# Optimization experiments

Measured on AMD Instinct MI355X. Metric: run time of the kernel, lower is better.

Reference implementation:

```python
import jax, jax.numpy as jnp
import numpy as np

SEQ_LEN, BATCH, HIDDEN, OUT = 512, 4096, 2048, 10


def setup_inputs() -> dict:
    key = jax.random.key(0)
    ks = jax.random.split(key, 7)
    return {
        "x": jax.random.normal(ks[0], (SEQ_LEN, BATCH), jnp.float32),
        "Wx": jax.random.normal(ks[1], (HIDDEN, 1), jnp.float32) * 0.05,
        "bx": jax.random.normal(ks[2], (HIDDEN,), jnp.float32) * 0.05,
        "Wh": jax.random.normal(ks[3], (1, HIDDEN), jnp.float32) * 0.05,
        "bh": jax.random.normal(ks[4], (1,), jnp.float32) * 0.05,
        "Wy": jax.random.normal(ks[5], (OUT, HIDDEN), jnp.float32) * 0.05,
        "by": jax.random.normal(ks[6], (OUT,), jnp.float32) * 0.05,
    }


def reference(x, Wx, bx, Wh, bh, Wy, by):
    # x: [T, B]; input_dim == 1 structurally (torch code reshapes x[i] to (B, 1)).
    B = x.shape[1]
    H = Wx.shape[0]
    wx = Wx[:, 0]  # [H]

    def step(h, xt):
        # linear_x(x_t): (B,1) @ (1,H) -> outer product, [B, H]
        x_out = xt[:, None] * wx[None, :] + bx
        # linear_h(h): [B, H] @ [H, 1] -> [B, 1], broadcasts into the add (as in torch)
        h_out = h @ Wh.T + bh
        h_new = jnp.tanh(x_out + h_out)
        return h_new, None

    h0 = jnp.zeros((B, H), x.dtype)
    h_final, _ = jax.lax.scan(step, h0, x)
    logits = h_final @ Wy.T + by  # [B, OUT]
    return jax.nn.softmax(logits, axis=-1)
```

## Files before the change

### kernel.cpp

```cpp
#include <hip/hip_runtime.h>
#include <math.h>


#define SEQ   512
#define BATCH 4096
#define HID   2048
#define NOUT  10
#define KPL   32
#define ROWQ  9

#define NS    560
#define S_LOc   (-10.0f)
#define S_H     (20.0f / 559.0f)
#define S_INVH  (559.0f / 20.0f)
#define S_BIAS  (10.0f * S_INVH)
#define NSM1F   559.0f
#define DZ14    43.0f
#define DZ9     69.875f
#define NSA     1120
#define NSAM1F  1119.0f
#define NSAM2F  1118.0f
#define S_HA    (20.0f / 1119.0f)
#define S_INVHA (1119.0f / 20.0f)
#define S_BIASA (10.0f * S_INVHA)
#define DZA     (1119.0f / 13.0f)
#define UPS_ALPHA (1119.0f / 559.0f)
#define U_SCALE (8.0f / 14.0f)
#define U_BIAS  4.0f
#define UCMAXF  7.99951f

#define TABLE_FLOATS (NS * ROWQ * 4)
#define WSA_FLOATS (4096 + 14 * 4096)
#define WSB_FLOATS (4096 + 4 * 4096)
#define WS3_FLOATS (57344 + 57344 + 4096 + 20160)

__device__ __forceinline__ float fast_exp2(float v) { return __builtin_amdgcn_exp2f(v); }
__device__ __forceinline__ float fast_rcp(float v)  { return __builtin_amdgcn_rcpf(v); }
__device__ __forceinline__ float med3(float a, float lo, float hi) {
    return __builtin_amdgcn_fmed3f(a, lo, hi);
}
__device__ __forceinline__ float fast_tanh(float a) {
    const float C = 2.8853900817779268f;
    return __builtin_fmaf(-2.0f, fast_rcp(fast_exp2(C * a) + 1.0f), 1.0f);
}
__device__ __forceinline__ float wave_sum(float v) {
#pragma unroll
    for (int m = 1; m < 64; m <<= 1) v += __shfl_xor(v, m, 64);
    return v;
}
__device__ __forceinline__ float combine_eval(float z, int nn, float dz,
                                              const float* baseA, const float* baseB,
                                              int split, int b) {
    float p = z / dz;
    int   c = min(max((int)floorf(p) - 1, 0), nn - 4);
    float t = p - (float)c;
    float a0 = t, a1 = t - 1.0f, a2 = t - 2.0f, a3 = t - 3.0f;
    float m01 = a0 * a1, m23 = a2 * a3;
    float w0 = a1 * m23 * (-1.0f / 6.0f), w1 = a0 * m23 * 0.5f;
    float w2 = m01 * a3 * (-0.5f),        w3 = m01 * a2 * (1.0f / 6.0f);
    float y[4];
#pragma unroll
    for (int i = 0; i < 4; ++i) {
        int n = c + i;
        const float* ptr = (n < split) ? (baseA + (size_t)n * 4096)
                                       : (baseB + (size_t)(n - split) * 4096);
        y[i] = ptr[b];
    }
    return __builtin_fmaf(w0, y[0], w1 * y[1]) + __builtin_fmaf(w2, y[2], w3 * y[3]);
}

__global__ __launch_bounds__(256) void k_coef(const float* __restrict__ Wx, const float* __restrict__ bx,
                                              const float* __restrict__ Wh, const float* __restrict__ bh,
                                              float* __restrict__ tab_g,
                                              float s_h, float s_invh, float s_bias) {
    __shared__ float red[256];
    __shared__ float Gn[32];
    const int k    = blockIdx.x;
    const int node = threadIdx.x & 31;
    const int jc   = threadIdx.x >> 5;
    const int cell = node >> 2, nn = node & 3;
    const float sn = S_LOc + (float)k * s_h;
    const float xi_n = (nn == 0) ? 0.923879533f : (nn == 1) ? 0.382683432f
                     : (nn == 2) ? -0.382683432f : -0.923879533f;
    const float un = (-7.0f + ((float)cell + 0.5f) * 1.75f) + 0.875f * xi_n;
    float p = 0.0f;
    const int j0 = jc * 256;
#pragma unroll 4
    for (int j = j0; j < j0 + 256; ++j)
        p += Wh[j] * fast_tanh(__builtin_fmaf(Wx[j], un, bx[j] + sn));
    red[threadIdx.x] = p;
    __syncthreads();
    if (threadIdx.x < 32) {
        float V = bh[0];
#pragma unroll
        for (int c = 0; c < 8; ++c) V += red[threadIdx.x + 32 * c];
        Gn[threadIdx.x] = __builtin_fmaf(V, s_invh, s_bias);
    }
    __syncthreads();
    float4* wq = (float4*)tab_g;
    if (threadIdx.x < 8) {
        const int c = threadIdx.x;
        float G0 = Gn[4*c+0], G1 = Gn[4*c+1], G2 = Gn[4*c+2], G3 = Gn[4*c+3];
        float d03 = G0 - G3, d12 = G1 - G2;
        float a0 = 0.25f * (G0 + G1 + G2 + G3);
        float a1 = 0.5f * (0.923879533f * d03 + 0.382683432f * d12);
        float a2 = 0.5f * 0.707106781f * (G0 - G1 - G2 + G3);
        float a3 = 0.5f * (0.382683432f * d03 - 0.923879533f * d12);
        wq[k * ROWQ + c] = make_float4(a0 - a2, a1 - 3.0f * a3, 2.0f * a2, 4.0f * a3);
    } else if (threadIdx.x == 8) {
        wq[k * ROWQ + 8] = make_float4(0.f, 0.f, 0.f, 0.f);
    }
}

__global__ __launch_bounds__(256) void k_upsample(const float* __restrict__ src,
                                                  float* __restrict__ dst) {
    const int idx = blockIdx.x * 256 + threadIdx.x;
    if (idx >= NSA * ROWQ) return;
    const int r = idx / 9;
    const int c = idx - r * 9;
    float4* d4 = (float4*)dst;
    if (c == 8) { d4[idx] = make_float4(0.f, 0.f, 0.f, 0.f); return; }
    float z5 = (float)r * (559.0f / 1119.0f);
    float kf = med3(floorf(z5) - 1.0f, 0.0f, 556.0f);
    int   k  = (int)kf;
    float t  = z5 - kf;
    float a0 = t, a1 = t - 1.0f, a2 = t - 2.0f, a3 = t - 3.0f;
    float m01 = a0 * a1, m23 = a2 * a3;
    float w0 = a1 * m23 * (-1.0f / 6.0f), w1 = a0 * m23 * 0.5f;
    float w2 = m01 * a3 * (-0.5f),        w3 = m01 * a2 * (1.0f / 6.0f);
    const float4* s4 = (const float4*)src;
    float4 y0 = s4[(k    ) * 9 + c];
    float4 y1 = s4[(k + 1) * 9 + c];
    float4 y2 = s4[(k + 2) * 9 + c];
    float4 y3 = s4[(k + 3) * 9 + c];
    float4 o;
    o.x = UPS_ALPHA * (w0 * y0.x + w1 * y1.x + w2 * y2.x + w3 * y3.x);
    o.y = UPS_ALPHA * (w0 * y0.y + w1 * y1.y + w2 * y2.y + w3 * y3.y);
    o.z = UPS_ALPHA * (w0 * y0.z + w1 * y1.z + w2 * y2.z + w3 * y3.z);
    o.w = UPS_ALPHA * (w0 * y0.w + w1 * y1.w + w2 * y2.w + w3 * y3.w);
    d4[idx] = o;
}

__global__ __launch_bounds__(256) void k_scan3(const float* __restrict__ x,
                                               const float* __restrict__ bh,
                                               const float* __restrict__ tab_g,
                                               float* __restrict__ z170,
                                               float* __restrict__ buf1,
                                               float* __restrict__ buf2) {
    __shared__ float4 tabs[NSA * ROWQ];
    {
        const float4* src = (const float4*)tab_g;
        for (int i = threadIdx.x; i < NSA * ROWQ; i += 256) tabs[i] = src[i];
    }
    __syncthreads();
    const int ptype = blockIdx.x >> 4;
    const int chunk = blockIdx.x & 15;
    const int b     = chunk * 256 + threadIdx.x;
    const int seg   = (ptype == 0) ? 0 : ((ptype <= 7) ? 1 : 2);
    const int nA    = (seg == 1) ? 2 * (ptype - 1) : ((seg == 2) ? 2 * (ptype - 8) : 0);
    const int nB    = nA + 1;

    const int t0     = (seg == 0) ? 0 : ((seg == 1) ? 170 : 340);
    const int nsteps = (seg == 2) ? 171 : 170;

    const float z0 = med3(__builtin_fmaf(bh[0], S_INVHA, S_BIASA), 0.0f, NSAM1F);
    float zA = (seg == 0) ? z0 : (float)nA * DZA;
    float zB = (seg == 0) ? z0 : (float)nB * DZA;

    auto step_pair = [&](float xi, float xi2, int ci) {
        float kfA = med3(zA, 0.0f, NSAM2F);
        float kfB = med3(zB, 0.0f, NSAM2F);
        int   kA  = (int)kfA;
        int   kB  = (int)kfB;
        int   ia  = ((kA << 3) + kA) + ci;
        int   ib  = ((kB << 3) + kB) + ci;
        float4 qa0 = tabs[ia];
        float4 qa1 = tabs[ia + ROWQ];
        float4 qb0 = tabs[ib];
        float4 qb1 = tabs[ib + ROWQ];
        float tA = med3(zA, 0.0f, NSAM1F) - (float)kA;
        float tB = med3(zB, 0.0f, NSAM1F) - (float)kB;
        float la0 = __builtin_fmaf(qa0.y, xi, qa0.x), ha0 = __builtin_fmaf(qa0.w, xi, qa0.z);
        float la1 = __builtin_fmaf(qa1.y, xi, qa1.x), ha1 = __builtin_fmaf(qa1.w, xi, qa1.z);
        float ra0 = __builtin_fmaf(ha0, xi2, la0);
        float ra1 = __builtin_fmaf(ha1, xi2, la1);
        zA = __builtin_fmaf(tA, ra1 - ra0, ra0);
        float lb0 = __builtin_fmaf(qb0.y, xi, qb0.x), hb0 = __builtin_fmaf(qb0.w, xi, qb0.z);
        float lb1 = __builtin_fmaf(qb1.y, xi, qb1.x), hb1 = __builtin_fmaf(qb1.w, xi, qb1.z);
        float rb0 = __builtin_fmaf(hb0, xi2, lb0);
        float rb1 = __builtin_fmaf(hb1, xi2, lb1);
        zB = __builtin_fmaf(tB, rb1 - rb0, rb0);
    };

    float cur[8], nxt[8];
#pragma unroll
    for (int i = 0; i < 8; ++i)
        cur[i] = x[(size_t)min(t0 + i, SEQ - 1) * BATCH + b];

    const int full = nsteps >> 3, tail = nsteps & 7;
    for (int c = 0; c < full; ++c) {
        const int nb = t0 + (c + 1) * 8;
#pragma unroll
        for (int i = 0; i < 8; ++i)
            nxt[i] = x[(size_t)min(nb + i, SEQ - 1) * BATCH + b];
        float xiA[8], xi2A[8]; int ciA[8];
#pragma unroll
        for (int i = 0; i < 8; ++i) {
            float uc = med3(__builtin_fmaf(cur[i], U_SCALE, U_BIAS), 0.0f, UCMAXF);
            int   ci = (int)uc;
            float xi = __builtin_fmaf(2.0f, uc - (float)ci, -1.0f);
            xiA[i] = xi; xi2A[i] = xi * xi; ciA[i] = ci;
        }
#pragma unroll
        for (int i = 0; i < 8; ++i) step_pair(xiA[i], xi2A[i], ciA[i]);
#pragma unroll
        for (int i = 0; i < 8; ++i) cur[i] = nxt[i];
    }
    for (int i = 0; i < tail; ++i) {
        float uc = med3(__builtin_fmaf(cur[i], U_SCALE, U_BIAS), 0.0f, UCMAXF);
        int   ci = (int)uc;
        float xi = __builtin_fmaf(2.0f, uc - (float)ci, -1.0f);
        step_pair(xi, xi * xi, ci);
    }

    if (seg == 0) {
        z170[b] = zA;
    } else if (seg == 1) {
        buf1[(size_t)nA * 4096 + b] = zA;
        buf1[(size_t)nB * 4096 + b] = zB;
    } else {
        buf2[(size_t)nA * 4096 + b] = zA;
        buf2[(size_t)nB * 4096 + b] = zB;
    }
}

__global__ __launch_bounds__(256) void head3(
    const float* __restrict__ x,  const float* __restrict__ Wx,
    const float* __restrict__ bx, const float* __restrict__ Wy,
    const float* __restrict__ by, const float* __restrict__ z170,
    const float* __restrict__ buf1, const float* __restrict__ buf2,
    float* __restrict__ out)
{
    const int lane = threadIdx.x & 63;
    const int wave = threadIdx.x >> 6;
    const int b    = blockIdx.x * 4 + wave;

    float z340 = combine_eval(z170[b], 14, DZA, buf1, buf1, 14, b);
    z340 = med3(z340, 0.0f, NSAM1F);
    float z511 = combine_eval(z340, 14, DZA, buf2, buf2, 14, b);
    const float s = __builtin_fmaf(z511, S_HA, S_LOc);

    const float C  = 2.8853900817779268f;
    const float u  = x[(size_t)(SEQ - 1) * BATCH + b];
    const float sc = s * C;
    float acc[NOUT];
#pragma unroll
    for (int i = 0; i < NOUT; ++i) acc[i] = 0.0f;
#pragma unroll 4
    for (int k = 0; k < KPL; ++k) {
        const int j = k * 64 + lane;
        float arg = __builtin_fmaf(u, Wx[j] * C, bx[j] * C) + sc;
        float r   = fast_rcp(fast_exp2(arg) + 1.0f);
        float th  = __builtin_fmaf(-2.0f, r, 1.0f);
#pragma unroll
        for (int i = 0; i < NOUT; ++i)
            acc[i] = __builtin_fmaf(Wy[i * HID + j], th, acc[i]);
    }
#pragma unroll
    for (int i = 0; i < NOUT; ++i) acc[i] = wave_sum(acc[i]) + by[i];
    float m = acc[0];
#pragma unroll
    for (int i = 1; i < NOUT; ++i) m = fmaxf(m, acc[i]);
    const float L2E = 1.4426950408889634f;
    float ev[NOUT]; float Z = 0.0f;
#pragma unroll
    for (int i = 0; i < NOUT; ++i) { ev[i] = fast_exp2((acc[i] - m) * L2E); Z += ev[i]; }
    const float rz = fast_rcp(Z);
    if (lane == 0) {
#pragma unroll
        for (int i = 0; i < NOUT; ++i) out[(size_t)b * NOUT + i] = ev[i] * rz;
    }
}

__global__ __launch_bounds__(256) void k_scan_quad(const float* __restrict__ x,
                                                   const float* __restrict__ bh,
                                                   const float* __restrict__ tab_g,
                                                   float* __restrict__ z255,
                                                   float* __restrict__ baseA,
                                                   float* __restrict__ baseB,
                                                   int split, float dz) {
    __shared__ float4 tabs[5200];
    {
        const float4* src = (const float4*)tab_g;
        for (int i = threadIdx.x; i < NS * ROWQ; i += 256) tabs[i] = src[i];
    }
    __syncthreads();
    const int blk = blockIdx.x;
    const int seg  = (blk < 16) ? 0 : 1;
    const int node = seg ? (blk - 16) >> 4 : 0;
    const int eb   = seg ? (blk - 16) & 15 : blk;
    const int b    = eb * 256 + threadIdx.x;

    const int t0     = seg ? 255 : 0;
    const int nsteps = seg ? 256 : 255;

    float za = seg ? (float)node * dz
                   : med3(__builtin_fmaf(bh[0], S_INVH, S_BIAS), 0.0f, NSM1F);

    auto step1 = [&](float xi, float xi2, int cim) {
        float mm  = med3(za + 0.5f, 1.0f, 558.0f);
        int   km  = (int)mm;
        int   idx = ((km << 3) + km) + cim;
        float4 qm = tabs[idx];
        float4 q0 = tabs[idx + ROWQ];
        float4 qp = tabs[idx + 2 * ROWQ];
        float kmf = (float)km;
        float zc  = med3(za, 0.0f, NSM1F);
        float t   = zc - kmf;
        float wm  = 0.5f * t * (t - 1.0f);
        float wp  = 0.5f * t * (t + 1.0f);
        float w0  = 1.0f - t * t;
        float lm = __builtin_fmaf(qm.y, xi, qm.x), hm = __builtin_fmaf(qm.w, xi, qm.z);
        float l0 = __builtin_fmaf(q0.y, xi, q0.x), h0 = __builtin_fmaf(q0.w, xi, q0.z);
        float lp = __builtin_fmaf(qp.y, xi, qp.x), hp = __builtin_fmaf(qp.w, xi, qp.z);
        float rm = __builtin_fmaf(hm, xi2, lm);
        float r0 = __builtin_fmaf(h0, xi2, l0);
        float rp = __builtin_fmaf(hp, xi2, lp);
        za = __builtin_fmaf(wm, rm, w0 * r0) + wp * rp;
    };

    float cur[8], nxt[8];
#pragma unroll
    for (int i = 0; i < 8; ++i)
        cur[i] = x[(size_t)min(t0 + i, SEQ - 1) * BATCH + b];

    const int full = nsteps >> 3, tail = nsteps & 7;
    for (int c = 0; c < full; ++c) {
        const int nb = t0 + (c + 1) * 8;
#pragma unroll
        for (int i = 0; i < 8; ++i)
            nxt[i] = x[(size_t)min(nb + i, SEQ - 1) * BATCH + b];
        float xiA[8], xi2A[8]; int cimA[8];
#pragma unroll
        for (int i = 0; i < 8; ++i) {
            float uc = med3(__builtin_fmaf(cur[i], U_SCALE, U_BIAS), 0.0f, UCMAXF);
            int   ci = (int)uc;
            float xi = __builtin_fmaf(2.0f, uc - (float)ci, -1.0f);
            xiA[i] = xi; xi2A[i] = xi * xi; cimA[i] = ci - ROWQ;
        }
#pragma unroll
        for (int i = 0; i < 8; ++i) step1(xiA[i], xi2A[i], cimA[i]);
#pragma unroll
        for (int i = 0; i < 8; ++i) cur[i] = nxt[i];
    }
    for (int i = 0; i < tail; ++i) {
        float uc = med3(__builtin_fmaf(cur[i], U_SCALE, U_BIAS), 0.0f, UCMAXF);
        int   ci = (int)uc;
        float xi = __builtin_fmaf(2.0f, uc - (float)ci, -1.0f);
        step1(xi, xi * xi, ci - ROWQ);
    }

    if (seg == 0) z255[b] = za;
    else {
        float* p = (node < split) ? (baseA + (size_t)node * 4096)
                                  : (baseB + (size_t)(node - split) * 4096);
        p[b] = za;
    }
}

__global__ __launch_bounds__(256) void k_combine(const float* __restrict__ baseA,
                                                 const float* __restrict__ baseB,
                                                 int split, int nn, float dz,
                                                 float* __restrict__ zs) {
    const int b = blockIdx.x * 256 + threadIdx.x;
    float zz = combine_eval(zs[b], nn, dz, baseA, baseB, split, b);
    zs[b] = __builtin_fmaf(zz, S_H, S_LOc);
}

__global__ __launch_bounds__(256) void head_combine_A(
    const float* __restrict__ x,  const float* __restrict__ Wx,
    const float* __restrict__ bx, const float* __restrict__ Wy,
    const float* __restrict__ by, const float* __restrict__ ws,
    float* __restrict__ out, float dz, float s_h)
{
    const int lane = threadIdx.x & 63;
    const int wave = threadIdx.x >> 6;
    const int b    = blockIdx.x * 4 + wave;

    float zz = combine_eval(ws[b], 14, dz, ws + 4096, ws + 4096, 14, b);
    const float s = __builtin_fmaf(zz, s_h, S_LOc);

    const float C  = 2.8853900817779268f;
    const float u  = x[(size_t)(SEQ - 1) * BATCH + b];
    const float sc = s * C;
    float acc[NOUT];
#pragma unroll
    for (int i = 0; i < NOUT; ++i) acc[i] = 0.0f;
#pragma unroll 4
    for (int k = 0; k < KPL; ++k) {
        const int j = k * 64 + lane;
        float arg = __builtin_fmaf(u, Wx[j] * C, bx[j] * C) + sc;
        float r   = fast_rcp(fast_exp2(arg) + 1.0f);
        float th  = __builtin_fmaf(-2.0f, r, 1.0f);
#pragma unroll
        for (int i = 0; i < NOUT; ++i)
            acc[i] = __builtin_fmaf(Wy[i * HID + j], th, acc[i]);
    }
#pragma unroll
    for (int i = 0; i < NOUT; ++i) acc[i] = wave_sum(acc[i]) + by[i];
    float m = acc[0];
#pragma unroll
    for (int i = 1; i < NOUT; ++i) m = fmaxf(m, acc[i]);
    const float L2E = 1.4426950408889634f;
    float ev[NOUT]; float Z = 0.0f;
#pragma unroll
    for (int i = 0; i < NOUT; ++i) { ev[i] = fast_exp2((acc[i] - m) * L2E); Z += ev[i]; }
    const float rz = fast_rcp(Z);
    if (lane == 0) {
#pragma unroll
        for (int i = 0; i < NOUT; ++i) out[(size_t)b * NOUT + i] = ev[i] * rz;
    }
}

__global__ __launch_bounds__(256) void rnn_scan_exact(
    const float* __restrict__ x,  const float* __restrict__ Wx,
    const float* __restrict__ bx, const float* __restrict__ Wh,
    const float* __restrict__ bh, float* __restrict__ s_out)
{
    const int lane = threadIdx.x & 63;
    const int wave = threadIdx.x >> 6;
    const int b    = blockIdx.x * 4 + wave;
    const float C = 2.8853900817779268f;
    float wxs[KPL], bxs[KPL], whn[KPL];
    float swh = 0.0f;
#pragma unroll
    for (int k = 0; k < KPL; ++k) {
        const int j = k * 64 + lane;
        const float w = Wh[j];
        wxs[k] = Wx[j] * C; bxs[k] = bx[j] * C; whn[k] = -2.0f * w; swh += w;
    }
    swh = wave_sum(swh);
    const float bh0 = bh[0];
    const float K0  = bh0 + swh;
    float s = bh0, u = x[b];
    for (int t = 0; t < SEQ - 1; ++t) {
        float u_next = x[(size_t)(t + 1) * BATCH + b];
        const float sc = s * C;
        float p = 0.0f;
#pragma unroll
        for (int k = 0; k < KPL; ++k) {
            float arg = __builtin_fmaf(u, wxs[k], bxs[k]) + sc;
            float r   = fast_rcp(fast_exp2(arg) + 1.0f);
            p = __builtin_fmaf(whn[k], r, p);
        }
        s = K0 + wave_sum(p);
        u = u_next;
    }
    if (lane == 0) s_out[b] = s;
}

__global__ __launch_bounds__(256) void rnn_head_exact(
    const float* __restrict__ x,  const float* __restrict__ Wx,
    const float* __restrict__ bx, const float* __restrict__ Wy,
    const float* __restrict__ by, const float* __restrict__ s_in,
    float* __restrict__ out)
{
    const int lane = threadIdx.x & 63;
    const int wave = threadIdx.x >> 6;
    const int b    = blockIdx.x * 4 + wave;
    const float C  = 2.8853900817779268f;
    const float s  = s_in[b];
    const float u  = x[(size_t)(SEQ - 1) * BATCH + b];
    const float sc = s * C;
    float acc[NOUT];
#pragma unroll
    for (int i = 0; i < NOUT; ++i) acc[i] = 0.0f;
#pragma unroll 4
    for (int k = 0; k < KPL; ++k) {
        const int j = k * 64 + lane;
        float arg = __builtin_fmaf(u, Wx[j] * C, bx[j] * C) + sc;
        float r   = fast_rcp(fast_exp2(arg) + 1.0f);
        float th  = __builtin_fmaf(-2.0f, r, 1.0f);
#pragma unroll
        for (int i = 0; i < NOUT; ++i)
            acc[i] = __builtin_fmaf(Wy[i * HID + j], th, acc[i]);
    }
#pragma unroll
    for (int i = 0; i < NOUT; ++i) acc[i] = wave_sum(acc[i]) + by[i];
    float m = acc[0];
#pragma unroll
    for (int i = 1; i < NOUT; ++i) m = fmaxf(m, acc[i]);
    const float L2E = 1.4426950408889634f;
    float ev[NOUT]; float Z = 0.0f;
#pragma unroll
    for (int i = 0; i < NOUT; ++i) { ev[i] = fast_exp2((acc[i] - m) * L2E); Z += ev[i]; }
    const float rz = fast_rcp(Z);
    if (lane == 0) {
#pragma unroll
        for (int i = 0; i < NOUT; ++i) out[(size_t)b * NOUT + i] = ev[i] * rz;
    }
}

extern "C" void kernel_launch(void* const* d_in, const int* in_sizes, int n_in,
                              void* d_out, int out_size, void* d_ws, size_t ws_size,
                              hipStream_t stream)
{
    const float* x  = (const float*)d_in[0];
    const float* Wx = (const float*)d_in[1];
    const float* bx = (const float*)d_in[2];
    const float* Wh = (const float*)d_in[3];
    const float* bh = (const float*)d_in[4];
    const float* Wy = (const float*)d_in[5];
    const float* by = (const float*)d_in[6];
    float* out = (float*)d_out;
    float* wf  = (float*)d_ws;

    if (ws_size >= (size_t)WS3_FLOATS * sizeof(float)) {
        float* buf1 = wf;
        float* buf2 = wf + 57344;
        float* z170 = wf + 114688;
        float* tmp5 = wf + 118784;
        k_coef<<<NS, 256, 0, stream>>>(Wx, bx, Wh, bh, tmp5, S_H, S_INVH, S_BIAS);
        k_upsample<<<(NSA * ROWQ + 255) / 256, 256, 0, stream>>>(tmp5, out);
        k_scan3<<<240, 256, 0, stream>>>(x, bh, out, z170, buf1, buf2);
        head3<<<BATCH / 4, 256, 0, stream>>>(x, Wx, bx, Wy, by, z170, buf1, buf2, out);
    } else if (ws_size >= (size_t)WSA_FLOATS * sizeof(float)) {
        k_coef<<<NS, 256, 0, stream>>>(Wx, bx, Wh, bh, out, S_H, S_INVH, S_BIAS);
        k_scan_quad<<<16 + 14 * 16, 256, 0, stream>>>(x, bh, out, wf,
                                                      wf + 4096, wf + 4096, 14, DZ14);
        head_combine_A<<<BATCH / 4, 256, 0, stream>>>(x, Wx, bx, Wy, by, wf, out,
                                                      DZ14, S_H);
    } else if (ws_size >= (size_t)WSB_FLOATS * sizeof(float)) {
        k_coef<<<NS, 256, 0, stream>>>(Wx, bx, Wh, bh, out, S_H, S_INVH, S_BIAS);
        k_scan_quad<<<16 + 9 * 16, 256, 0, stream>>>(x, bh, out, wf,
                                                     out + TABLE_FLOATS, wf + 4096, 5, DZ9);
        k_combine<<<16, 256, 0, stream>>>(out + TABLE_FLOATS, wf + 4096, 5, 9, DZ9, wf);
        rnn_head_exact<<<BATCH / 4, 256, 0, stream>>>(x, Wx, bx, Wy, by, wf, out);
    } else {
        rnn_scan_exact<<<BATCH / 4, 256, 0, stream>>>(x, Wx, bx, Wh, bh, wf);
        rnn_head_exact<<<BATCH / 4, 256, 0, stream>>>(x, Wx, bx, Wy, by, wf, out);
    }
}
```

Measured before the change: 134.1 us.

## Split scan into four time segments with ten sampled start states each

```diff
diff --git a/kernel.cpp b/kernel.cpp
--- a/kernel.cpp
+++ b/kernel.cpp
@@ -24,6 +24,7 @@
 #define S_INVHA (1119.0f / 20.0f)
 #define S_BIASA (10.0f * S_INVHA)
 #define DZA     (1119.0f / 13.0f)
+#define DZ10    (1119.0f / 9.0f)
 #define UPS_ALPHA (1119.0f / 559.0f)
 #define U_SCALE (8.0f / 14.0f)
 #define U_BIAS  4.0f
@@ -33,6 +34,7 @@
 #define WSA_FLOATS (4096 + 14 * 4096)
 #define WSB_FLOATS (4096 + 4 * 4096)
 #define WS3_FLOATS (57344 + 57344 + 4096 + 20160)
+#define WS4_FLOATS (3 * 40960 + 4096 + 20160)
 
 __device__ __forceinline__ float fast_exp2(float v) { return __builtin_amdgcn_exp2f(v); }
 __device__ __forceinline__ float fast_rcp(float v)  { return __builtin_amdgcn_rcpf(v); }
@@ -141,12 +143,13 @@
     d4[idx] = o;
 }
 
-__global__ __launch_bounds__(256) void k_scan3(const float* __restrict__ x,
+__global__ __launch_bounds__(256) void k_scan4(const float* __restrict__ x,
                                                const float* __restrict__ bh,
                                                const float* __restrict__ tab_g,
-                                               float* __restrict__ z170,
+                                               float* __restrict__ z128,
                                                float* __restrict__ buf1,
-                                               float* __restrict__ buf2) {
+                                               float* __restrict__ buf2,
+                                               float* __restrict__ buf3) {
     __shared__ float4 tabs[NSA * ROWQ];
     {
         const float4* src = (const float4*)tab_g;
@@ -156,16 +159,19 @@
     const int ptype = blockIdx.x >> 4;
     const int chunk = blockIdx.x & 15;
     const int b     = chunk * 256 + threadIdx.x;
-    const int seg   = (ptype == 0) ? 0 : ((ptype <= 7) ? 1 : 2);
-    const int nA    = (seg == 1) ? 2 * (ptype - 1) : ((seg == 2) ? 2 * (ptype - 8) : 0);
-    const int nB    = nA + 1;
-
-    const int t0     = (seg == 0) ? 0 : ((seg == 1) ? 170 : 340);
-    const int nsteps = (seg == 2) ? 171 : 170;
+    int seg, nA;
+    if      (ptype == 0)  { seg = 0; nA = 0; }
+    else if (ptype <= 5)  { seg = 1; nA = 2 * (ptype - 1); }
+    else if (ptype <= 10) { seg = 2; nA = 2 * (ptype - 6); }
+    else                  { seg = 3; nA = 2 * (ptype - 11); }
+    const int nB = nA + 1;
+
+    const int t0     = seg * 128;
+    const int nsteps = (seg == 3) ? 127 : 128;
 
     const float z0 = med3(__builtin_fmaf(bh[0], S_INVHA, S_BIASA), 0.0f, NSAM1F);
-    float zA = (seg == 0) ? z0 : (float)nA * DZA;
-    float zB = (seg == 0) ? z0 : (float)nB * DZA;
+    float zA = (seg == 0) ? z0 : (float)nA * DZ10;
+    float zB = (seg == 0) ? z0 : (float)nB * DZ10;
 
     auto step_pair = [&](float xi, float xi2, int ci) {
         float kfA = med3(zA, 0.0f, NSAM2F);
@@ -224,6 +230,147 @@
     }
 
     if (seg == 0) {
+        z128[b] = zA;
+    } else {
+        float* buf = (seg == 1) ? buf1 : ((seg == 2) ? buf2 : buf3);
+        buf[(size_t)nA * 4096 + b] = zA;
+        buf[(size_t)nB * 4096 + b] = zB;
+    }
+}
+
+__global__ __launch_bounds__(256) void head4(
+    const float* __restrict__ x,  const float* __restrict__ Wx,
+    const float* __restrict__ bx, const float* __restrict__ Wy,
+    const float* __restrict__ by, const float* __restrict__ z128,
+    const float* __restrict__ buf1, const float* __restrict__ buf2,
+    const float* __restrict__ buf3, float* __restrict__ out)
+{
+    const int lane = threadIdx.x & 63;
+    const int wave = threadIdx.x >> 6;
+    const int b    = blockIdx.x * 4 + wave;
+
+    float z = combine_eval(z128[b], 10, DZ10, buf1, buf1, 10, b);
+    z = med3(z, 0.0f, NSAM1F);
+    z = combine_eval(z, 10, DZ10, buf2, buf2, 10, b);
+    z = med3(z, 0.0f, NSAM1F);
+    z = combine_eval(z, 10, DZ10, buf3, buf3, 10, b);
+    const float s = __builtin_fmaf(z, S_HA, S_LOc);
+
+    const float C  = 2.8853900817779268f;
+    const float u  = x[(size_t)(SEQ - 1) * BATCH + b];
+    const float sc = s * C;
+    float acc[NOUT];
+#pragma unroll
+    for (int i = 0; i < NOUT; ++i) acc[i] = 0.0f;
+#pragma unroll 4
+    for (int k = 0; k < KPL; ++k) {
+        const int j = k * 64 + lane;
+        float arg = __builtin_fmaf(u, Wx[j] * C, bx[j] * C) + sc;
+        float r   = fast_rcp(fast_exp2(arg) + 1.0f);
+        float th  = __builtin_fmaf(-2.0f, r, 1.0f);
+#pragma unroll
+        for (int i = 0; i < NOUT; ++i)
+            acc[i] = __builtin_fmaf(Wy[i * HID + j], th, acc[i]);
+    }
+#pragma unroll
+    for (int i = 0; i < NOUT; ++i) acc[i] = wave_sum(acc[i]) + by[i];
+    float m = acc[0];
+#pragma unroll
+    for (int i = 1; i < NOUT; ++i) m = fmaxf(m, acc[i]);
+    const float L2E = 1.4426950408889634f;
+    float ev[NOUT]; float Z = 0.0f;
+#pragma unroll
+    for (int i = 0; i < NOUT; ++i) { ev[i] = fast_exp2((acc[i] - m) * L2E); Z += ev[i]; }
+    const float rz = fast_rcp(Z);
+    if (lane == 0) {
+#pragma unroll
+        for (int i = 0; i < NOUT; ++i) out[(size_t)b * NOUT + i] = ev[i] * rz;
+    }
+}
+
+__global__ __launch_bounds__(256) void k_scan3(const float* __restrict__ x,
+                                               const float* __restrict__ bh,
+                                               const float* __restrict__ tab_g,
+                                               float* __restrict__ z170,
+                                               float* __restrict__ buf1,
+                                               float* __restrict__ buf2) {
+    __shared__ float4 tabs[NSA * ROWQ];
+    {
+        const float4* src = (const float4*)tab_g;
+        for (int i = threadIdx.x; i < NSA * ROWQ; i += 256) tabs[i] = src[i];
+    }
+    __syncthreads();
+    const int ptype = blockIdx.x >> 4;
+    const int chunk = blockIdx.x & 15;
+    const int b     = chunk * 256 + threadIdx.x;
+    const int seg   = (ptype == 0) ? 0 : ((ptype <= 7) ? 1 : 2);
+    const int nA    = (seg == 1) ? 2 * (ptype - 1) : ((seg == 2) ? 2 * (ptype - 8) : 0);
+    const int nB    = nA + 1;
+
+    const int t0     = (seg == 0) ? 0 : ((seg == 1) ? 170 : 340);
+    const int nsteps = (seg == 2) ? 171 : 170;
+
+    const float z0 = med3(__builtin_fmaf(bh[0], S_INVHA, S_BIASA), 0.0f, NSAM1F);
+    float zA = (seg == 0) ? z0 : (float)nA * DZA;
+    float zB = (seg == 0) ? z0 : (float)nB * DZA;
+
+    auto step_pair = [&](float xi, float xi2, int ci) {
+        float kfA = med3(zA, 0.0f, NSAM2F);
+        float kfB = med3(zB, 0.0f, NSAM2F);
+        int   kA  = (int)kfA;
+        int   kB  = (int)kfB;
+        int   ia  = ((kA << 3) + kA) + ci;
+        int   ib  = ((kB << 3) + kB) + ci;
+        float4 qa0 = tabs[ia];
+        float4 qa1 = tabs[ia + ROWQ];
+        float4 qb0 = tabs[ib];
+        float4 qb1 = tabs[ib + ROWQ];
+        float tA = med3(zA, 0.0f, NSAM1F) - (float)kA;
+        float tB = med3(zB, 0.0f, NSAM1F) - (float)kB;
+        float la0 = __builtin_fmaf(qa0.y, xi, qa0.x), ha0 = __builtin_fmaf(qa0.w, xi, qa0.z);
+        float la1 = __builtin_fmaf(qa1.y, xi, qa1.x), ha1 = __builtin_fmaf(qa1.w, xi, qa1.z);
+        float ra0 = __builtin_fmaf(ha0, xi2, la0);
+        float ra1 = __builtin_fmaf(ha1, xi2, la1);
+        zA = __builtin_fmaf(tA, ra1 - ra0, ra0);
+        float lb0 = __builtin_fmaf(qb0.y, xi, qb0.x), hb0 = __builtin_fmaf(qb0.w, xi, qb0.z);
+        float lb1 = __builtin_fmaf(qb1.y, xi, qb1.x), hb1 = __builtin_fmaf(qb1.w, xi, qb1.z);
+        float rb0 = __builtin_fmaf(hb0, xi2, lb0);
+        float rb1 = __builtin_fmaf(hb1, xi2, lb1);
+        zB = __builtin_fmaf(tB, rb1 - rb0, rb0);
+    };
+
+    float cur[8], nxt[8];
+#pragma unroll
+    for (int i = 0; i < 8; ++i)
+        cur[i] = x[(size_t)min(t0 + i, SEQ - 1) * BATCH + b];
+
+    const int full = nsteps >> 3, tail = nsteps & 7;
+    for (int c = 0; c < full; ++c) {
+        const int nb = t0 + (c + 1) * 8;
+#pragma unroll
+        for (int i = 0; i < 8; ++i)
+            nxt[i] = x[(size_t)min(nb + i, SEQ - 1) * BATCH + b];
+        float xiA[8], xi2A[8]; int ciA[8];
+#pragma unroll
+        for (int i = 0; i < 8; ++i) {
+            float uc = med3(__builtin_fmaf(cur[i], U_SCALE, U_BIAS), 0.0f, UCMAXF);
+            int   ci = (int)uc;
+            float xi = __builtin_fmaf(2.0f, uc - (float)ci, -1.0f);
+            xiA[i] = xi; xi2A[i] = xi * xi; ciA[i] = ci;
+        }
+#pragma unroll
+        for (int i = 0; i < 8; ++i) step_pair(xiA[i], xi2A[i], ciA[i]);
+#pragma unroll
+        for (int i = 0; i < 8; ++i) cur[i] = nxt[i];
+    }
+    for (int i = 0; i < tail; ++i) {
+        float uc = med3(__builtin_fmaf(cur[i], U_SCALE, U_BIAS), 0.0f, UCMAXF);
+        int   ci = (int)uc;
+        float xi = __builtin_fmaf(2.0f, uc - (float)ci, -1.0f);
+        step_pair(xi, xi * xi, ci);
+    }
+
+    if (seg == 0) {
         z170[b] = zA;
     } else if (seg == 1) {
         buf1[(size_t)nA * 4096 + b] = zA;
@@ -515,7 +662,18 @@
     float* out = (float*)d_out;
     float* wf  = (float*)d_ws;
 
-    if (ws_size >= (size_t)WS3_FLOATS * sizeof(float)) {
+    if (ws_size >= (size_t)WS4_FLOATS * sizeof(float)) {
+        float* buf1 = wf;
+        float* buf2 = wf + 40960;
+        float* buf3 = wf + 81920;
+        float* z128 = wf + 122880;
+        float* tmp5 = wf + 126976;
+        k_coef<<<NS, 256, 0, stream>>>(Wx, bx, Wh, bh, tmp5, S_H, S_INVH, S_BIAS);
+        k_upsample<<<(NSA * ROWQ + 255) / 256, 256, 0, stream>>>(tmp5, out);
+        k_scan4<<<256, 256, 0, stream>>>(x, bh, out, z128, buf1, buf2, buf3);
+        head4<<<BATCH / 4, 256, 0, stream>>>(x, Wx, bx, Wy, by, z128,
+                                             buf1, buf2, buf3, out);
+    } else if (ws_size >= (size_t)WS3_FLOATS * sizeof(float)) {
         float* buf1 = wf;
         float* buf2 = wf + 57344;
         float* z170 = wf + 114688;
```

After: 129.0 us. -3.8%, faster.
